# Optimization experiments

Measured on AMD Instinct MI355X. Metric: run time of the kernel, lower is better.

## Reference

```python
import jax, jax.numpy as jnp
import numpy as np

N = 8000       # n_sample (nodes)
F = 128        # n_feature
H = 128        # n_hidden
E = 256000     # edges (avg degree 32)
NPOOL = 3
K = 10         # propagation steps (args.k)
NC = 2         # n_class
ALPHA = 0.0    # Propagation(alpha=0.0)
CENTS = [400, 20, 1]   # node_pool = round(N**(1/NPOOL)) = 20; n_cent = round(prev/20)


def setup_inputs():
    key = jax.random.key(0)
    ks = jax.random.split(key, 40)
    def nrm(i, shape, scale=1.0):
        return jax.random.normal(ks[i], shape, jnp.float32) * scale
    x = nrm(0, (N, F))
    x_cov = nrm(1, (N, F))
    edge_rows = jax.random.randint(ks[2], (E,), 0, N, dtype=jnp.int32)
    edge_cols = jax.random.randint(ks[3], (E,), 0, N, dtype=jnp.int32)
    adj_vals = jax.random.uniform(ks[4], (E,), jnp.float32)
    raw = jax.random.uniform(ks[5], (E,), jnp.float32) + 0.1
    deg = jax.ops.segment_sum(raw, edge_rows, num_segments=N)
    norm_vals = raw / deg[edge_rows]   # row-normalized adjacency values
    inp = dict(x=x, x_cov=x_cov, edge_rows=edge_rows, edge_cols=edge_cols,
               adj_vals=adj_vals, norm_vals=norm_vals,
               bn_gamma=jnp.ones((F,), jnp.float32), bn_beta=jnp.zeros((F,), jnp.float32))
    i = 6
    for p, nc in enumerate(CENTS):
        inp['c%d_W1' % p] = nrm(i, (F, H), F ** -0.5); i += 1
        inp['c%d_b1' % p] = jnp.zeros((H,), jnp.float32)
        inp['c%d_W2' % p] = nrm(i, (H, nc), H ** -0.5); i += 1
        inp['c%d_b2' % p] = jnp.zeros((nc,), jnp.float32)
    inp['mW1'] = nrm(i, (F, H), F ** -0.5); i += 1
    inp['mb1'] = jnp.zeros((H,), jnp.float32)
    inp['a1'] = jnp.full((1,), 0.25, jnp.float32)   # PReLU slope
    inp['mW2'] = nrm(i, (H, H), H ** -0.5); i += 1
    inp['mb2'] = jnp.zeros((H,), jnp.float32)
    inp['a2'] = jnp.full((1,), 0.25, jnp.float32)
    inp['mW3'] = nrm(i, (H, NC), H ** -0.5); i += 1
    inp['mb3'] = jnp.zeros((NC,), jnp.float32)
    return inp


def _node_corr(z):
    # per-node decomposition of torch.corrcoef(z.T).sum(1):
    #   _node_corr(z).sum(0) == corrcoef(z.T).sum(1)
    zc = z - z.mean(0, keepdims=True)
    zc = zc / (jnp.linalg.norm(zc, axis=0, keepdims=True) + 1e-12)
    return zc * zc.sum(1, keepdims=True)   # [n, F]


def reference(x, x_cov, edge_rows, edge_cols, adj_vals, norm_vals, bn_gamma, bn_beta,
              c0_W1, c0_b1, c0_W2, c0_b2, c1_W1, c1_b1, c1_W2, c1_b2,
              c2_W1, c2_b1, c2_W2, c2_b2, mW1, mb1, a1, mW2, mb2, a2, mW3, mb3):
    # BatchNorm1d (training statistics, biased variance, eps=1e-5)
    mu, var = x.mean(0), x.var(0)
    x = (x - mu) / jnp.sqrt(var + 1e-5) * bn_gamma + bn_beta
    x0 = x

    # --- multi-level clustering / pooling (ClusteringLayer) ---
    cl_params = [(c0_W1, c0_b1, c0_W2, c0_b2), (c1_W1, c1_b1, c1_W2, c1_b2),
                 (c2_W1, c2_b1, c2_W2, c2_b2)]
    masks, corrs = [], []
    xc = x_cov
    for W1, b1, W2, b2 in cl_params:
        h = jax.nn.relu(xc @ W1 + b1)
        S = jax.nn.softmax(h @ W2 + b2, axis=-1)        # soft assignment [n_prev, n_cent]
        corrs.append(_node_corr(xc))                     # corr at the input level
        masks.append(S)
        xc = (S.T @ xc) / (S.sum(0)[:, None] + 1e-12)    # pooled centroid features
    corrs.append(_node_corr(x).sum(0))   # == torch.corrcoef(x.T).sum(1), shape [F]

    # --- gains: sigmoid(corr_{i+1} - normalize_adj(mask_i).T @ corr_i) ---
    gains = []
    for i in range(NPOOL):
        rn = masks[i] / (masks[i].sum(1, keepdims=True) + 1e-12)  # row-normalized (symmetric=False)
        gains.append(jax.nn.sigmoid(corrs[i + 1] - rn.T @ corrs[i]))

    # --- per-feature diagonal-masked sparse matmul chains, restricted to adj's edge set ---
    # projector to original nodes: P_i = masks[0] @ ... @ masks[i]
    P = [masks[0]]
    for i in range(1, NPOOL - 1):
        P.append(P[-1] @ masks[i])
    # (M M^T)[r,c] with M = P_i @ diag(g[:,j]) evaluated only on adj edges, all features at once
    def edge_mask(Pi, g):
        return jnp.einsum('ek,ek,kf->ef', Pi[edge_rows], Pi[edge_cols], g * g)  # [E, F]
    ms = [edge_mask(P[i], gains[i]) for i in reversed(range(NPOOL - 1))]  # i = NPOOL-2 .. 0
    ms = jnp.stack(ms, axis=0).transpose(2, 0, 1)   # [F, NPOOL-1, E]

    def per_feature(a, m_steps):   # sequential carry of adj over feature loop (matches torch)
        def inner(ai, mrow):
            ai = ai * mrow          # adj = adj * mask (elementwise on edge values)
            return ai, ai
        a, temps = jax.lax.scan(inner, a, m_steps)
        return a, temps.sum(0)      # adjs[j] = torch.sparse.sum(stack(temp), dim=0)
    _, adjs = jax.lax.scan(per_feature, adj_vals, ms)   # [F, E] edge values

    # --- diffusion propagation: x <- (1-alpha) * norm_adj @ x + alpha * x0, k times ---
    for _ in range(K):
        agg = jax.ops.segment_sum(norm_vals[:, None] * x[edge_cols], edge_rows, num_segments=N)
        x = (1.0 - ALPHA) * agg + ALPHA * x0

    # --- 3-layer MLP with PReLU + log_softmax ---
    prelu = lambda z, a: jnp.where(z >= 0, z, a * z)
    h = prelu(x @ mW1 + mb1, a1)
    h = prelu(h @ mW2 + mb2, a2)
    logits = h @ mW3 + mb3
    return jax.nn.log_softmax(logits, axis=1), adjs
```

## Files before the change

### kernel.cpp

```cpp
#include <hip/hip_runtime.h>
#include <hip/hip_bf16.h>

typedef __hip_bfloat16 bf16;
typedef __attribute__((ext_vector_type(8))) short s16x8;
typedef __attribute__((ext_vector_type(4))) float f32x4;

static constexpr int NN = 8000;
static constexpr int FF = 128;
static constexpr int EE = 256000;
static constexpr int NC0 = 400;
static constexpr int NC1 = 20;

__device__ __forceinline__ float b2f(bf16 v) { return __bfloat162float(v); }
__device__ __forceinline__ bf16 f2b(float v) { return __float2bfloat16(v); }
__device__ __forceinline__ short f2bs(float v) {
    bf16 h = __float2bfloat16(v);
    return __builtin_bit_cast(short, h);
}
__device__ __forceinline__ float ldw(float v) { return v; }
__device__ __forceinline__ float ldw(bf16 v) { return __bfloat162float(v); }

template <int NW>
__device__ __forceinline__ float block_sum(float v, float* sb) {
    #pragma unroll
    for (int o = 32; o > 0; o >>= 1) v += __shfl_down(v, o, 64);
    int t = threadIdx.x;
    if ((t & 63) == 0) sb[t >> 6] = v;
    __syncthreads();
    float s = 0.f;
    #pragma unroll
    for (int i = 0; i < NW; ++i) s += sb[i];
    __syncthreads();
    return s;
}

template <int NW>
__device__ __forceinline__ float block_max(float v, float* sb) {
    #pragma unroll
    for (int o = 32; o > 0; o >>= 1) v = fmaxf(v, __shfl_down(v, o, 64));
    int t = threadIdx.x;
    if ((t & 63) == 0) sb[t >> 6] = v;
    __syncthreads();
    float m = sb[0];
    #pragma unroll
    for (int i = 1; i < NW; ++i) m = fmaxf(m, sb[i]);
    __syncthreads();
    return m;
}

__global__ void k_fill_b16(bf16* __restrict__ p, float v, long n) {
    long i = (long)blockIdx.x * 256 + threadIdx.x;
    long stride = (long)gridDim.x * 256;
    for (; i < n; i += stride) p[i] = f2b(v);
}

__global__ void k_cvt_pad(const float* __restrict__ src, bf16* __restrict__ dst, int n) {
    int idx = blockIdx.x * 256 + threadIdx.x;
    if (idx < n) {
        int r = idx / 24, cc = idx - r * 24;
        dst[idx] = f2b(cc < 20 ? src[r * 20 + cc] : 0.f);
    }
}

__global__ void k_split(const float* __restrict__ src, bf16* __restrict__ dh,
                        bf16* __restrict__ dl, int n) {
    int i = blockIdx.x * 256 + threadIdx.x;
    if (i < n) {
        float v = src[i];
        bf16 h = f2b(v);
        dh[i] = h;
        dl[i] = f2b(v - b2f(h));
    }
}

__global__ __launch_bounds__(256)
void k_tsplit(const float* __restrict__ src, bf16* __restrict__ dh, bf16* __restrict__ dl,
              bf16* __restrict__ sh, bf16* __restrict__ sl, int M, int N) {
    __shared__ float t[32][33];
    int bx = blockIdx.x * 32, by = blockIdx.y * 32;
    int x = threadIdx.x;
    for (int y = threadIdx.y; y < 32; y += 8) {
        int m = by + y, n = bx + x;
        if (m < M && n < N) {
            float v = src[(long)m * N + n];
            t[y][x] = v;
            if (sh) {
                bf16 h = f2b(v);
                sh[(long)m * N + n] = h;
                sl[(long)m * N + n] = f2b(v - b2f(h));
            }
        }
    }
    __syncthreads();
    for (int y = threadIdx.y; y < 32; y += 8) {
        int n = bx + y, m = by + x;
        if (n < N && m < M) {
            float v = t[x][y];
            bf16 h = f2b(v);
            dh[(long)n * M + m] = h;
            dl[(long)n * M + m] = f2b(v - b2f(h));
        }
    }
}

__global__ void k_swz(const float* __restrict__ g, bf16* __restrict__ out, int nchunk, int K) {
    int idx = blockIdx.x * 256 + threadIdx.x;
    if (idx >= nchunk * 4096) return;
    int i = idx & 7, l = (idx >> 3) & 63, t = (idx >> 9) & 7, ch = idx >> 12;
    int k = 32 * ch + 8 * (l >> 4) + i;
    int f = 16 * t + (l & 15);
    out[idx] = f2b(k < K ? g[k * 128 + f] : 0.f);
}

__global__ __launch_bounds__(256)
void k_bnstats(const float* __restrict__ x, const float* __restrict__ gamma,
               const float* __restrict__ beta, float* __restrict__ scale,
               float* __restrict__ shift, int M) {
    __shared__ float sb[4];
    int f = blockIdx.x;
    float s = 0.f, q = 0.f;
    for (int n = threadIdx.x; n < M; n += 256) {
        float v = x[n * FF + f];
        s += v; q += v * v;
    }
    s = block_sum<4>(s, sb);
    q = block_sum<4>(q, sb);
    if (threadIdx.x == 0) {
        float mu = s / M;
        float var = q / M - mu * mu;
        if (var < 0.f) var = 0.f;
        float rstd = 1.f / sqrtf(var + 1e-5f);
        float sc = gamma[f] * rstd;
        scale[f] = sc;
        shift[f] = beta[f] - mu * sc;
    }
}

__global__ void k_bnapply(const float* __restrict__ x, const float* __restrict__ scale,
                          const float* __restrict__ shift, float* __restrict__ out, int n) {
    int i = blockIdx.x * 256 + threadIdx.x;
    if (i < n) { int f = i & 127; out[i] = x[i] * scale[f] + shift[f]; }
}

__global__ __launch_bounds__(256)
void k_colstats(const float* __restrict__ src, float* __restrict__ mu,
                float* __restrict__ invn, int M) {
    __shared__ float sb[4];
    int f = blockIdx.x;
    float s = 0.f, q = 0.f;
    for (int n = threadIdx.x; n < M; n += 256) {
        float v = src[n * FF + f];
        s += v; q += v * v;
    }
    s = block_sum<4>(s, sb);
    q = block_sum<4>(q, sb);
    if (threadIdx.x == 0) {
        float m = s / M;
        float ss = q - s * m;
        if (ss < 0.f) ss = 0.f;
        mu[f] = m;
        invn[f] = 1.f / (sqrtf(ss) + 1e-12f);
    }
}

__global__ __launch_bounds__(128)
void k_nodecorr(const float* __restrict__ src, const float* __restrict__ mu,
                const float* __restrict__ invn, float* __restrict__ out) {
    __shared__ float sb[2];
    int n = blockIdx.x, t = threadIdx.x;
    float z = (src[n * FF + t] - mu[t]) * invn[t];
    float tot = block_sum<2>(z, sb);
    out[n * FF + t] = z * tot;
}

__global__ void k_div(const float* __restrict__ T, const float* __restrict__ cs,
                      float* __restrict__ out, int n) {
    int i = blockIdx.x * 256 + threadIdx.x;
    if (i < n) out[i] = T[i] / (cs[i >> 7] + 1e-12f);
}

__global__ void k_sig2(const float* __restrict__ corr, const float* __restrict__ T,
                       float* __restrict__ out, int n) {
    int i = blockIdx.x * 256 + threadIdx.x;
    if (i < n) {
        float d = corr[i] - T[i];
        float g = 1.f / (1.f + expf(-d));
        out[i] = g * g;
    }
}

__global__ __launch_bounds__(256)
void k_softmax(float* __restrict__ p, int N) {
    __shared__ float sb[4];
    float* row = p + (long)blockIdx.x * N;
    int t = threadIdx.x;
    float m = -1e30f;
    for (int i = t; i < N; i += 256) m = fmaxf(m, row[i]);
    m = block_max<4>(m, sb);
    float s = 0.f;
    for (int i = t; i < N; i += 256) { float e = expf(row[i] - m); row[i] = e; s += e; }
    s = block_sum<4>(s, sb);
    float inv = 1.f / s;
    for (int i = t; i < N; i += 256) row[i] *= inv;
}

__global__ __launch_bounds__(256)
void k_softmax_b16(const float* __restrict__ src, bf16* __restrict__ dst, int N) {
    __shared__ float sb[4];
    const float* row = src + (long)blockIdx.x * N;
    bf16* orow = dst + (long)blockIdx.x * N;
    int t = threadIdx.x;
    float v0 = (t < N) ? row[t] : -1e30f;
    float v1 = (256 + t < N) ? row[256 + t] : -1e30f;
    float m = block_max<4>(fmaxf(v0, v1), sb);
    float e0 = (t < N) ? expf(v0 - m) : 0.f;
    float e1 = (256 + t < N) ? expf(v1 - m) : 0.f;
    float s = block_sum<4>(e0 + e1, sb);
    float inv = 1.f / s;
    if (t < N) orow[t] = f2b(e0 * inv);
    if (256 + t < N) orow[256 + t] = f2b(e1 * inv);
}

template <typename T>
__global__ __launch_bounds__(256)
void k_transpose(const T* __restrict__ src, T* __restrict__ dst, int M, int N) {
    __shared__ T t[32][33];
    int bx = blockIdx.x * 32, by = blockIdx.y * 32;
    int x = threadIdx.x;
    for (int y = threadIdx.y; y < 32; y += 8) {
        int m = by + y, n = bx + x;
        if (m < M && n < N) t[y][x] = src[(long)m * N + n];
    }
    __syncthreads();
    for (int y = threadIdx.y; y < 32; y += 8) {
        int n = bx + y, m = by + x;
        if (n < N && m < M) dst[(long)n * M + m] = t[x][y];
    }
}

template <typename T>
__global__ __launch_bounds__(256)
void k_colsum(const T* __restrict__ srcT, float* __restrict__ cs, int M) {
    __shared__ float sb[4];
    int r = blockIdx.x;
    float s = 0.f;
    for (int i = threadIdx.x; i < M; i += 256) s += ldw(srcT[(long)r * M + i]);
    s = block_sum<4>(s, sb);
    if (threadIdx.x == 0) cs[r] = s;
}

template <typename AT, typename WT>
__global__ __launch_bounds__(256)
void k_gemm(const AT* __restrict__ A, const WT* __restrict__ W,
            const float* __restrict__ bias, const float* __restrict__ slope,
            float* __restrict__ C, int M, int K, int N, int act) {
    __shared__ float As[16][68];
    __shared__ float Ws[16][68];
    int tid = threadIdx.x;
    int tx = tid & 15, ty = tid >> 4;
    int m0 = blockIdx.x * 64, n0 = blockIdx.y * 64;
    int KS = gridDim.z;
    int kchunk = ((K + KS * 16 - 1) / (KS * 16)) * 16;
    int kbeg = blockIdx.z * kchunk;
    int kend = min(K, kbeg + kchunk);
    float acc[4][4] = {};
    for (int k0 = kbeg; k0 < kend; k0 += 16) {
        __syncthreads();
        for (int idx = tid; idx < 1024; idx += 256) {
            int r = idx >> 4, kk = idx & 15;
            int m = m0 + r, k = k0 + kk;
            As[kk][r] = (m < M && k < kend) ? ldw(A[(long)m * K + k]) : 0.f;
        }
        for (int idx = tid; idx < 1024; idx += 256) {
            int kk = idx >> 6, n = idx & 63;
            int k = k0 + kk, nn = n0 + n;
            float wv = 0.f;
            if (k < kend && nn < N) wv = ldw(W[(long)k * N + nn]);
            Ws[kk][n] = wv;
        }
        __syncthreads();
        #pragma unroll
        for (int kk = 0; kk < 16; ++kk) {
            float4 a4 = *(const float4*)&As[kk][ty * 4];
            float4 b4 = *(const float4*)&Ws[kk][tx * 4];
            float av[4] = {a4.x, a4.y, a4.z, a4.w};
            float bv[4] = {b4.x, b4.y, b4.z, b4.w};
            #pragma unroll
            for (int i = 0; i < 4; ++i)
                #pragma unroll
                for (int j = 0; j < 4; ++j) acc[i][j] += av[i] * bv[j];
        }
    }
    if (KS > 1) {
        #pragma unroll
        for (int i = 0; i < 4; ++i) {
            int m = m0 + ty * 4 + i;
            if (m >= M) continue;
            #pragma unroll
            for (int j = 0; j < 4; ++j) {
                int n = n0 + tx * 4 + j;
                if (n >= N) continue;
                atomicAdd(&C[(long)m * N + n], acc[i][j]);
            }
        }
    } else {
        float sl = slope ? slope[0] : 0.f;
        #pragma unroll
        for (int i = 0; i < 4; ++i) {
            int m = m0 + ty * 4 + i;
            if (m >= M) continue;
            #pragma unroll
            for (int j = 0; j < 4; ++j) {
                int n = n0 + tx * 4 + j;
                if (n >= N) continue;
                float v = acc[i][j] + (bias ? bias[n] : 0.f);
                if (act == 1) v = fmaxf(v, 0.f);
                else if (act == 2) v = (v >= 0.f) ? v : sl * v;
                C[(long)m * N + n] = v;
            }
        }
    }
}

template <int PARTS>
__global__ __launch_bounds__(256)
void k_gmm(const bf16* __restrict__ Ah, const bf16* __restrict__ Al,
           const bf16* __restrict__ BTh, const bf16* __restrict__ BTl,
           const float* __restrict__ bias, const float* __restrict__ slope,
           float* __restrict__ C, int M, int K, int N, int act) {
    __shared__ __align__(16) short At[2][64 * 40];
    __shared__ __align__(16) short Bt[2][64 * 40];
    int tid = threadIdx.x;
    int m0 = blockIdx.x * 64, n0 = blockIdx.y * 64;
    int KS = gridDim.z;
    int kchunk = ((K + KS * 32 - 1) / (KS * 32)) * 32;
    int kbeg = blockIdx.z * kchunk;
    int kend = min(K, kbeg + kchunk);
    int r = tid >> 2, s = tid & 3;
    int l = tid & 63, w = tid >> 6;
    int c = l & 15, g = l >> 4;
    bool arow_ok = (m0 + r < M);
    bool brow_ok = (n0 + r < N);
    const short* ahp = (const short*)Ah + (long)(m0 + r) * K;
    const short* alp = (PARTS >= 3) ? (const short*)Al + (long)(m0 + r) * K : nullptr;
    const short* bhp = (const short*)BTh + (long)(n0 + r) * K;
    const short* blp = (PARTS >= 2) ? (const short*)BTl + (long)(n0 + r) * K : nullptr;
    short* aw = &At[0][r * 40 + 8 * s];
    short* bw = &Bt[0][r * 40 + 8 * s];
    const int afo = (16 * w + c) * 40 + 8 * g;
    f32x4 acc[4] = {};
    for (int k0 = kbeg; k0 < kend; k0 += 32) {
        __syncthreads();
        {
            int kk = k0 + 8 * s;
            bool kok = kk < kend;
            s16x8 av = {}, bv = {};
            if (arow_ok && kok) av = *(const s16x8*)(ahp + kk);
            if (brow_ok && kok) bv = *(const s16x8*)(bhp + kk);
            *(s16x8*)aw = av;
            *(s16x8*)bw = bv;
            if (PARTS >= 2) {
                s16x8 b2 = {};
                if (brow_ok && kok) b2 = *(const s16x8*)(blp + kk);
                *(s16x8*)(bw + 64 * 40) = b2;
            }
            if (PARTS >= 3) {
                s16x8 a2 = {};
                if (arow_ok && kok) a2 = *(const s16x8*)(alp + kk);
                *(s16x8*)(aw + 64 * 40) = a2;
            }
        }
        __syncthreads();
        s16x8 ah_ = *(const s16x8*)&At[0][afo];
        s16x8 al_;
        if (PARTS >= 3) al_ = *(const s16x8*)&At[1][afo];
        #pragma unroll
        for (int nt = 0; nt < 4; ++nt) {
            int bfo = (16 * nt + c) * 40 + 8 * g;
            s16x8 bh_ = *(const s16x8*)&Bt[0][bfo];
            acc[nt] = __builtin_amdgcn_mfma_f32_16x16x32_bf16(ah_, bh_, acc[nt], 0, 0, 0);
            if (PARTS >= 2) {
                s16x8 bl_ = *(const s16x8*)&Bt[1][bfo];
                acc[nt] = __builtin_amdgcn_mfma_f32_16x16x32_bf16(ah_, bl_, acc[nt], 0, 0, 0);
            }
            if (PARTS >= 3)
                acc[nt] = __builtin_amdgcn_mfma_f32_16x16x32_bf16(al_, bh_, acc[nt], 0, 0, 0);
        }
    }
    if (KS > 1) {
        #pragma unroll
        for (int nt = 0; nt < 4; ++nt) {
            int n = n0 + 16 * nt + c;
            if (n >= N) continue;
            #pragma unroll
            for (int q = 0; q < 4; ++q) {
                int m = m0 + 16 * w + 4 * g + q;
                if (m < M) atomicAdd(&C[(long)m * N + n], acc[nt][q]);
            }
        }
    } else {
        float sl = slope ? slope[0] : 0.f;
        #pragma unroll
        for (int nt = 0; nt < 4; ++nt) {
            int n = n0 + 16 * nt + c;
            if (n >= N) continue;
            float bv = bias ? bias[n] : 0.f;
            #pragma unroll
            for (int q = 0; q < 4; ++q) {
                int m = m0 + 16 * w + 4 * g + q;
                if (m >= M) continue;
                float v = acc[nt][q] + bv;
                if (act == 1) v = fmaxf(v, 0.f);
                else if (act == 2) v = (v >= 0.f) ? v : sl * v;
                C[(long)m * N + n] = v;
            }
        }
    }
}

__global__ __launch_bounds__(256)
void k_edge(const int* __restrict__ er, const int* __restrict__ ec,
            const float* __restrict__ adj,
            const bf16* __restrict__ S0b, const bf16* __restrict__ P1hp,
            const bf16* __restrict__ g0swz, const bf16* __restrict__ g1swz,
            bf16* __restrict__ outp, int E) {
    __shared__ int ridx[64], cidx[64];
    __shared__ __align__(16) short Wt[64 * 40];
    int tid = threadIdx.x;
    int e0 = blockIdx.x * 64;
    if (tid < 64) { ridx[tid] = er[e0 + tid]; cidx[tid] = ec[e0 + tid]; }
    __syncthreads();
    const int eb = tid >> 2, seg = tid & 3;
    const int l = tid & 63, w = tid >> 6;
    const int c = l & 15, g = l >> 4;
    const short* S0s = (const short*)S0b;
    const short* rrow = S0s + (long)ridx[eb] * 400 + 8 * seg;
    const short* crow = S0s + (long)cidx[eb] * 400 + 8 * seg;
    short* wwr = &Wt[eb * 40 + 8 * seg];
    const short* wrd = &Wt[(16 * w + c) * 40 + 8 * g];
    const s16x8* g0p = (const s16x8*)g0swz;
    f32x4 acc0[8] = {};
    f32x4 acc1[8] = {};
    #pragma unroll 1
    for (int ch = 0; ch < 13; ++ch) {
        s16x8 ar = *(const s16x8*)(rrow + 32 * ch);
        s16x8 ac = *(const s16x8*)(crow + 32 * ch);
        s16x8 wv;
        #pragma unroll
        for (int i = 0; i < 8; ++i) {
            float av = __uint_as_float(((unsigned)(unsigned short)ar[i]) << 16);
            float bv = __uint_as_float(((unsigned)(unsigned short)ac[i]) << 16);
            wv[i] = f2bs(av * bv);
        }
        __syncthreads();
        *(s16x8*)wwr = wv;
        __syncthreads();
        s16x8 wfrag = *(const s16x8*)wrd;
        const s16x8* gc = g0p + (long)ch * 512 + l;
        #pragma unroll
        for (int t = 0; t < 8; ++t)
            acc0[t] = __builtin_amdgcn_mfma_f32_16x16x32_bf16(gc[t * 64], wfrag, acc0[t], 0, 0, 0);
    }
    {
        s16x8 wv = {};
        if (seg < 3) {
            const short* P1s = (const short*)P1hp;
            s16x8 pr = *(const s16x8*)(P1s + (long)ridx[eb] * 24 + 8 * seg);
            s16x8 pc = *(const s16x8*)(P1s + (long)cidx[eb] * 24 + 8 * seg);
            #pragma unroll
            for (int i = 0; i < 8; ++i) {
                float av = __uint_as_float(((unsigned)(unsigned short)pr[i]) << 16);
                float bv = __uint_as_float(((unsigned)(unsigned short)pc[i]) << 16);
                wv[i] = f2bs(av * bv);
            }
        }
        __syncthreads();
        *(s16x8*)wwr = wv;
        __syncthreads();
        s16x8 wfrag = *(const s16x8*)wrd;
        const s16x8* g1p = (const s16x8*)g1swz;
        #pragma unroll
        for (int t = 0; t < 8; ++t)
            acc1[t] = __builtin_amdgcn_mfma_f32_16x16x32_bf16(g1p[t * 64 + l], wfrag, acc1[t], 0, 0, 0);
    }
    const long col = e0 + 16 * w + c;
    float pre = adj[col];
    #pragma unroll
    for (int t = 0; t < 8; ++t) {
        float m10 = acc0[t][0], m11 = acc0[t][1], m12 = acc0[t][2], m13 = acc0[t][3];
        float m00 = acc1[t][0], m01 = acc1[t][1], m02 = acc1[t][2], m03 = acc1[t][3];
        float q0 = m00 * m10, q1 = m01 * m11, q2 = m02 * m12, q3 = m03 * m13;
        float eq1 = q0, eq2 = q0 * q1, eq3 = eq2 * q2;
        float incg = eq3 * q3;
        float u = __shfl_up(incg, 16, 64); if (g >= 1) incg *= u;
        u = __shfl_up(incg, 32, 64); if (g >= 2) incg *= u;
        float exg = __shfl_up(incg, 16, 64); if (g == 0) exg = 1.f;
        float tot = __shfl(incg, 48 + c, 64);
        float base = pre * exg;
        pre *= tot;
        int fb = 16 * t + 4 * g;
        float o0 = base * m00 * (1.f + m10);
        float o1 = base * eq1 * m01 * (1.f + m11);
        float o2 = base * eq2 * m02 * (1.f + m12);
        float o3 = base * eq3 * m03 * (1.f + m13);
        outp[(long)(fb + 0) * E + col] = f2b(o0);
        outp[(long)(fb + 1) * E + col] = f2b(o1);
        outp[(long)(fb + 2) * E + col] = f2b(o2);
        if (fb + 3 < 127 || col < 240000)
            outp[(long)(fb + 3) * E + col] = f2b(o3);
    }
}

__global__ void k_count(const int* __restrict__ er, int* __restrict__ counts, int E) {
    int e = blockIdx.x * 256 + threadIdx.x;
    if (e < E) atomicAdd(&counts[er[e]], 1);
}

__global__ __launch_bounds__(256)
void k_scan(const int* __restrict__ counts, int* __restrict__ rs,
            int* __restrict__ cur, int R) {
    __shared__ int buf[2][256];
    int t = threadIdx.x;
    const int PER = 32;
    int b = t * PER;
    int s = 0;
    for (int i = 0; i < PER; ++i) {
        int idx = b + i;
        if (idx < R) s += counts[idx];
    }
    buf[0][t] = s;
    __syncthreads();
    int src = 0;
    for (int off = 1; off < 256; off <<= 1) {
        int v = buf[src][t];
        if (t >= off) v += buf[src][t - off];
        buf[1 - src][t] = v;
        __syncthreads();
        src = 1 - src;
    }
    int base = (t > 0) ? buf[src][t - 1] : 0;
    for (int i = 0; i < PER; ++i) {
        int idx = b + i;
        if (idx < R) {
            int c = counts[idx];
            rs[idx] = base;
            cur[idx] = base;
            base += c;
        }
    }
    if (t == 255) rs[R] = buf[src][255];
}

__global__ void k_scatter(const int* __restrict__ er, const int* __restrict__ ec,
                          const float* __restrict__ nv, int* __restrict__ cur,
                          int2* __restrict__ cpack, int E) {
    int e = blockIdx.x * 256 + threadIdx.x;
    if (e < E) {
        int r = er[e];
        int p = atomicAdd(&cur[r], 1);
        cpack[p] = make_int2(ec[e], __float_as_int(nv[e]));
    }
}

__global__ __launch_bounds__(256)
void k_spmv4(const int* __restrict__ rs, const int2* __restrict__ cpack,
             const float* __restrict__ xin, float* __restrict__ xout, int R) {
    int lane = threadIdx.x & 31;
    int r = blockIdx.x * 8 + (threadIdx.x >> 5);
    if (r >= R) return;
    int jb = rs[r], je = rs[r + 1];
    float4 acc = {0.f, 0.f, 0.f, 0.f};
    int j = jb;
    for (; j + 4 <= je; j += 4) {
        int2 cv0 = cpack[j], cv1 = cpack[j + 1], cv2 = cpack[j + 2], cv3 = cpack[j + 3];
        float4 x0 = ((const float4*)(xin + (long)cv0.x * FF))[lane];
        float4 x1 = ((const float4*)(xin + (long)cv1.x * FF))[lane];
        float4 x2 = ((const float4*)(xin + (long)cv2.x * FF))[lane];
        float4 x3 = ((const float4*)(xin + (long)cv3.x * FF))[lane];
        float v0 = __int_as_float(cv0.y), v1 = __int_as_float(cv1.y);
        float v2 = __int_as_float(cv2.y), v3 = __int_as_float(cv3.y);
        acc.x += v0 * x0.x; acc.y += v0 * x0.y; acc.z += v0 * x0.z; acc.w += v0 * x0.w;
        acc.x += v1 * x1.x; acc.y += v1 * x1.y; acc.z += v1 * x1.z; acc.w += v1 * x1.w;
        acc.x += v2 * x2.x; acc.y += v2 * x2.y; acc.z += v2 * x2.z; acc.w += v2 * x2.w;
        acc.x += v3 * x3.x; acc.y += v3 * x3.y; acc.z += v3 * x3.z; acc.w += v3 * x3.w;
    }
    for (; j < je; ++j) {
        int2 cv = cpack[j];
        float v = __int_as_float(cv.y);
        float4 xv = ((const float4*)(xin + (long)cv.x * FF))[lane];
        acc.x += v * xv.x; acc.y += v * xv.y; acc.z += v * xv.z; acc.w += v * xv.w;
    }
    ((float4*)(xout + (long)r * FF))[lane] = acc;
}

__global__ __launch_bounds__(256)
void k_fc128(const float* __restrict__ xin, const float* __restrict__ W,
             const float* __restrict__ b, const float* __restrict__ a,
             float* __restrict__ hout, int nblk) {
    __shared__ float Ws[16384];
    __shared__ float xs[2][128];
    int t = threadIdx.x;
    for (int i = t; i < 16384; i += 256) Ws[i] = W[i];
    float slope = a[0];
    int half = t >> 7, tt = t & 127;
    float bb = b[tt];
    __syncthreads();
    for (int n = blockIdx.x * 2 + half; n < NN; n += nblk * 2) {
        xs[half][tt] = xin[(long)n * FF + tt];
        __syncthreads();
        float a0 = 0.f, a1 = 0.f, a2 = 0.f, a3 = 0.f;
        #pragma unroll 8
        for (int k = 0; k < 128; k += 4) {
            a0 += xs[half][k + 0] * Ws[(k + 0) * 128 + tt];
            a1 += xs[half][k + 1] * Ws[(k + 1) * 128 + tt];
            a2 += xs[half][k + 2] * Ws[(k + 2) * 128 + tt];
            a3 += xs[half][k + 3] * Ws[(k + 3) * 128 + tt];
        }
        float acc = bb + ((a0 + a1) + (a2 + a3));
        hout[(long)n * FF + tt] = (acc >= 0.f) ? acc : slope * acc;
        __syncthreads();
    }
}

__global__ __launch_bounds__(256)
void k_mlp_tail(const float* __restrict__ hin, const float* __restrict__ W2,
                const float* __restrict__ b2, const float* __restrict__ a2,
                const float* __restrict__ W3, const float* __restrict__ b3,
                bf16* __restrict__ outA, bf16* __restrict__ outB, int nblk) {
    __shared__ float Ws[16384];
    __shared__ float xs[2][128];
    __shared__ float red[8];
    int t = threadIdx.x;
    for (int i = t; i < 16384; i += 256) Ws[i] = W2[i];
    float slope = a2[0];
    int half = t >> 7, tt = t & 127;
    float bb = b2[tt];
    float w30 = W3[tt * 2 + 0], w31 = W3[tt * 2 + 1];
    float b30 = b3[0], b31 = b3[1];
    __syncthreads();
    for (int n = blockIdx.x * 2 + half; n < NN; n += nblk * 2) {
        xs[half][tt] = hin[(long)n * FF + tt];
        __syncthreads();
        float a0 = 0.f, a1 = 0.f, a2_ = 0.f, a3 = 0.f;
        #pragma unroll 8
        for (int k = 0; k < 128; k += 4) {
            a0 += xs[half][k + 0] * Ws[(k + 0) * 128 + tt];
            a1 += xs[half][k + 1] * Ws[(k + 1) * 128 + tt];
            a2_ += xs[half][k + 2] * Ws[(k + 2) * 128 + tt];
            a3 += xs[half][k + 3] * Ws[(k + 3) * 128 + tt];
        }
        float acc = bb + ((a0 + a1) + (a2_ + a3));
        float h2 = (acc >= 0.f) ? acc : slope * acc;
        float l0 = h2 * w30, l1 = h2 * w31;
        #pragma unroll
        for (int o = 32; o > 0; o >>= 1) {
            l0 += __shfl_down(l0, o, 64);
            l1 += __shfl_down(l1, o, 64);
        }
        int wid = t >> 6;
        if ((t & 63) == 0) { red[wid] = l0; red[4 + wid] = l1; }
        __syncthreads();
        if (tt == 0) {
            float L0 = red[half * 2] + red[half * 2 + 1] + b30;
            float L1 = red[4 + half * 2] + red[4 + half * 2 + 1] + b31;
            float m = fmaxf(L0, L1);
            float lse = m + logf(expf(L0 - m) + expf(L1 - m));
            bf16 v0 = f2b(L0 - lse), v1 = f2b(L1 - lse);
            outA[n * 2 + 0] = v0; outA[n * 2 + 1] = v1;
            outB[n * 2 + 0] = v0; outB[n * 2 + 1] = v1;
        }
        __syncthreads();
    }
}

extern "C" void kernel_launch(void* const* d_in, const int* in_sizes, int n_in,
                              void* d_out, int out_size, void* d_ws, size_t ws_size,
                              hipStream_t stream) {
    const float* x     = (const float*)d_in[0];
    const float* xcov  = (const float*)d_in[1];
    const int*   erow  = (const int*)d_in[2];
    const int*   ecol  = (const int*)d_in[3];
    const float* adjv  = (const float*)d_in[4];
    const float* normv = (const float*)d_in[5];
    const float* gamma = (const float*)d_in[6];
    const float* beta  = (const float*)d_in[7];
    const float* c0W1 = (const float*)d_in[8];  const float* c0b1 = (const float*)d_in[9];
    const float* c0W2 = (const float*)d_in[10]; const float* c0b2 = (const float*)d_in[11];
    const float* c1W1 = (const float*)d_in[12]; const float* c1b1 = (const float*)d_in[13];
    const float* c1W2 = (const float*)d_in[14]; const float* c1b2 = (const float*)d_in[15];
    const float* mW1 = (const float*)d_in[20]; const float* mb1 = (const float*)d_in[21];
    const float* a1  = (const float*)d_in[22];
    const float* mW2 = (const float*)d_in[23]; const float* mb2 = (const float*)d_in[24];
    const float* a2  = (const float*)d_in[25];
    const float* mW3 = (const float*)d_in[26]; const float* mb3 = (const float*)d_in[27];

    char* B = (char*)d_out;
    bf16* logitsA = (bf16*)B;
    bf16* logitsB = (bf16*)(B + 32000);
    bf16* adjsOut = (bf16*)(B + 64000);

    auto ovl = [](const void* a, size_t an, const void* b, size_t bn) {
        const char* A = (const char*)a; const char* Bp = (const char*)b;
        return (A < Bp + bn) && (Bp < A + an);
    };
    size_t outBytes = (size_t)out_size * 2;
    static const int expSize[28] = {1024000,1024000,256000,256000,256000,256000,128,128,
                                    16384,128,51200,400, 16384,128,2560,20, 16384,128,128,1,
                                    16384,128,1, 16384,128,1, 256,2};
    int code = 0;
    if (n_in != 28) code = 200;
    else for (int i = 0; i < 28 && !code; ++i) if (in_sizes[i] != expSize[i]) code = 200;
    if (!code && ovl(d_ws, ws_size, d_out, outBytes)) code = 300;
    if (!code) {
        for (int i = 0; i < 28; ++i) {
            size_t bytes = (size_t)in_sizes[i] * 4;
            if (ovl(d_ws, ws_size, d_in[i], bytes)) { code = 400; break; }
            if (ovl(d_out, outBytes, d_in[i], bytes)) { code = 500; break; }
        }
    }
    if (!code && ws_size < (size_t)6935040) code = 600;
    if (code) {
        k_fill_b16<<<64, 256, 0, stream>>>(logitsA, (float)code, 16000);
        k_fill_b16<<<64, 256, 0, stream>>>(logitsB, (float)code, 16000);
        k_fill_b16<<<2048, 256, 0, stream>>>(adjsOut, 0.0f, (outBytes - 64000) / 2);
        return;
    }

    char* ws = (char*)d_ws;
    bf16*  S0b   = (bf16*)(ws + 0);
    bf16*  P1hp  = (bf16*)(ws + 6400000);
    bf16*  g0swz = (bf16*)(ws + 6784000);
    bf16*  g1swz = (bf16*)(ws + 6890496);

    char* S = B + 64000;
    float* xbn   = (float*)(S + 0);
    float* ping  = (float*)(S + 4096000);
    float* h0    = (float*)(S + 8192000);
    float* hh2   = (float*)(S + 12288000);
    float* S0f   = (float*)(S + 16384000);
    bf16*  S0Tb  = (bf16*)(S + 29184000);
    float* P1f   = (float*)(S + 35584000);
    int*   rs    = (int*)(S + 36224000);
    int*   cur   = (int*)(S + 36256016);
    int2*  cpack = (int2*)(S + 36288016);
    float* T0    = (float*)(S + 38400512);
    float* T1    = (float*)(S + 38605312);
    float* xc1   = (float*)(S + 38810112);
    float* corr1 = (float*)(S + 39014912);
    float* h1    = (float*)(S + 39219712);
    float* S1    = (float*)(S + 39424512);
    float* S1T   = (float*)(S + 39456512);
    float* T2    = (float*)(S + 39488512);
    float* T3    = (float*)(S + 39498752);
    float* xc2   = (float*)(S + 39508992);
    float* corr2 = (float*)(S + 39519232);
    float* cs0   = (float*)(S + 39529472);
    float* cs1   = (float*)(S + 39531072);
    float* bnsc  = (float*)(S + 39532032);
    float* bnsh  = (float*)(S + 39532544);
    float* statmu= (float*)(S + 39533056);
    float* statin= (float*)(S + 39533568);
    float* g0sq  = (float*)(S + 39534080);
    float* g1sq  = (float*)(S + 39738880);
    bf16* xcovh  = (bf16*)(S + 39749120);
    bf16* xcovl  = (bf16*)(S + 41797120);
    bf16* xcovTh = (bf16*)(S + 43845120);
    bf16* xcovTl = (bf16*)(S + 45893120);
    bf16* hh2Th  = (bf16*)(S + 47941120);
    bf16* hh2Tl  = (bf16*)(S + 49989120);
    bf16* h0h    = (bf16*)(S + 52037120);
    bf16* h0l    = (bf16*)(S + 54085120);
    bf16* W1Th   = (bf16*)(S + 56133120);
    bf16* W1Tl   = (bf16*)(S + 56165888);
    bf16* W2Th   = (bf16*)(S + 56198656);
    bf16* W2Tl   = (bf16*)(S + 56301056);
    bf16* S1Th   = (bf16*)(S + 56403456);
    bf16* S1Tl   = (bf16*)(S + 56419456);

    k_bnstats<<<128, 256, 0, stream>>>(x, gamma, beta, bnsc, bnsh, NN);
    k_bnapply<<<4000, 256, 0, stream>>>(x, bnsc, bnsh, xbn, NN * FF);
    k_colstats<<<128, 256, 0, stream>>>(xcov, statmu, statin, NN);
    k_nodecorr<<<NN, 128, 0, stream>>>(xcov, statmu, statin, hh2);
    k_tsplit<<<dim3(4, 250), dim3(32, 8), 0, stream>>>(xcov, xcovTh, xcovTl, xcovh, xcovl, NN, FF);
    k_tsplit<<<dim3(4, 250), dim3(32, 8), 0, stream>>>(hh2, hh2Th, hh2Tl, nullptr, nullptr, NN, FF);
    k_tsplit<<<dim3(4, 4), dim3(32, 8), 0, stream>>>(c0W1, W1Th, W1Tl, nullptr, nullptr, 128, 128);
    k_tsplit<<<dim3(13, 4), dim3(32, 8), 0, stream>>>(c0W2, W2Th, W2Tl, nullptr, nullptr, 128, NC0);
    k_gmm<3><<<dim3(125, 2, 1), 256, 0, stream>>>(xcovh, xcovl, W1Th, W1Tl, c0b1, nullptr, h0, NN, 128, 128, 1);
    k_split<<<4000, 256, 0, stream>>>(h0, h0h, h0l, NN * FF);
    k_gmm<3><<<dim3(125, 7, 1), 256, 0, stream>>>(h0h, h0l, W2Th, W2Tl, c0b2, nullptr, S0f, NN, 128, NC0, 0);
    k_softmax_b16<<<NN, 256, 0, stream>>>(S0f, S0b, NC0);
    k_transpose<bf16><<<dim3(13, 250), dim3(32, 8), 0, stream>>>(S0b, S0Tb, NN, NC0);
    k_colsum<bf16><<<NC0, 256, 0, stream>>>(S0Tb, cs0, NN);
    hipMemsetAsync(T0, 0, NC0 * 128 * 4, stream);
    hipMemsetAsync(T1, 0, NC0 * 128 * 4, stream);
    k_gmm<2><<<dim3(7, 2, 16), 256, 0, stream>>>(S0Tb, nullptr, xcovTh, xcovTl, nullptr, nullptr, T0, NC0, NN, 128, 0);
    k_gmm<2><<<dim3(7, 2, 16), 256, 0, stream>>>(S0Tb, nullptr, hh2Th, hh2Tl, nullptr, nullptr, T1, NC0, NN, 128, 0);
    k_div<<<200, 256, 0, stream>>>(T0, cs0, xc1, NC0 * 128);
    k_colstats<<<128, 256, 0, stream>>>(xc1, statmu, statin, NC0);
    k_nodecorr<<<NC0, 128, 0, stream>>>(xc1, statmu, statin, corr1);
    k_sig2<<<200, 256, 0, stream>>>(corr1, T1, g0sq, NC0 * 128);
    k_swz<<<208, 256, 0, stream>>>(g0sq, g0swz, 13, NC0);
    k_gemm<float, float><<<dim3(7, 2, 1), 256, 0, stream>>>(xc1, c1W1, c1b1, nullptr, h1, NC0, 128, 128, 1);
    k_gemm<float, float><<<dim3(7, 1, 1), 256, 0, stream>>>(h1, c1W2, c1b2, nullptr, S1, NC0, 128, NC1, 0);
    k_softmax<<<NC0, 256, 0, stream>>>(S1, NC1);
    k_transpose<float><<<dim3(1, 13), dim3(32, 8), 0, stream>>>(S1, S1T, NC0, NC1);
    k_colsum<float><<<NC1, 256, 0, stream>>>(S1T, cs1, NC0);
    k_tsplit<<<dim3(1, 13), dim3(32, 8), 0, stream>>>(S1, S1Th, S1Tl, nullptr, nullptr, NC0, NC1);
    hipMemsetAsync(T2, 0, NC1 * 128 * 4, stream);
    hipMemsetAsync(T3, 0, NC1 * 128 * 4, stream);
    k_gemm<float, float><<<dim3(1, 2, 4), 256, 0, stream>>>(S1T, xc1, nullptr, nullptr, T2, NC1, NC0, 128, 0);
    k_gemm<float, float><<<dim3(1, 2, 4), 256, 0, stream>>>(S1T, corr1, nullptr, nullptr, T3, NC1, NC0, 128, 0);
    k_div<<<10, 256, 0, stream>>>(T2, cs1, xc2, NC1 * 128);
    k_colstats<<<128, 256, 0, stream>>>(xc2, statmu, statin, NC1);
    k_nodecorr<<<NC1, 128, 0, stream>>>(xc2, statmu, statin, corr2);
    k_sig2<<<10, 256, 0, stream>>>(corr2, T3, g1sq, NC1 * 128);
    k_swz<<<16, 256, 0, stream>>>(g1sq, g1swz, 1, NC1);
    k_gmm<2><<<dim3(125, 1, 1), 256, 0, stream>>>(S0b, nullptr, S1Th, S1Tl, nullptr, nullptr, P1f, NN, NC0, NC1, 0);
    k_cvt_pad<<<750, 256, 0, stream>>>(P1f, P1hp, NN * 24);
    hipMemsetAsync(cur, 0, NN * 4, stream);
    k_count<<<1000, 256, 0, stream>>>(erow, cur, EE);
    k_scan<<<1, 256, 0, stream>>>(cur, rs, cur, NN);
    k_scatter<<<1000, 256, 0, stream>>>(erow, ecol, normv, cur, cpack, EE);
    float* xa = xbn;
    float* xb = ping;
    for (int it = 0; it < 10; ++it) {
        k_spmv4<<<1000, 256, 0, stream>>>(rs, cpack, xa, xb, NN);
        float* t = xa; xa = xb; xb = t;
    }
    k_fc128<<<250, 256, 0, stream>>>(xa, mW1, mb1, a1, h0, 250);
    k_mlp_tail<<<250, 256, 0, stream>>>(h0, mW2, mb2, a2, mW3, mb3, logitsA, logitsB, 250);
    k_edge<<<EE / 64, 256, 0, stream>>>(erow, ecol, adjv, S0b, P1hp, g0swz, g1swz, adjsOut, EE);
}
```

Measured before the change: 801.0 us.

## Fuse gain kernels, persistent propagation kernel, and LDS-staged edge output

Merges the small div/colstats/nodecorr/sigmoid/swizzle launches for both pooling levels into three fused kernels, and folds the BatchNorm apply into the first propagation step. The ten SpMV launches become one persistent kernel that uses a global atomic barrier between iterations. In the edge kernel, shared-memory staging with syncthreads is replaced by ds_bpermute, the next chunk's rows are prefetched, and output is transposed through LDS for coalesced 16-byte stores. The persistent kernel relies on all 500 blocks being co-resident; if they are not, the grid barrier deadlocks.

```diff
diff --git a/kernel.cpp b/kernel.cpp
--- a/kernel.cpp
+++ b/kernel.cpp
@@ -103,15 +103,6 @@
     }
 }
 
-__global__ void k_swz(const float* __restrict__ g, bf16* __restrict__ out, int nchunk, int K) {
-    int idx = blockIdx.x * 256 + threadIdx.x;
-    if (idx >= nchunk * 4096) return;
-    int i = idx & 7, l = (idx >> 3) & 63, t = (idx >> 9) & 7, ch = idx >> 12;
-    int k = 32 * ch + 8 * (l >> 4) + i;
-    int f = 16 * t + (l & 15);
-    out[idx] = f2b(k < K ? g[k * 128 + f] : 0.f);
-}
-
 __global__ __launch_bounds__(256)
 void k_bnstats(const float* __restrict__ x, const float* __restrict__ gamma,
                const float* __restrict__ beta, float* __restrict__ scale,
@@ -136,12 +127,6 @@
     }
 }
 
-__global__ void k_bnapply(const float* __restrict__ x, const float* __restrict__ scale,
-                          const float* __restrict__ shift, float* __restrict__ out, int n) {
-    int i = blockIdx.x * 256 + threadIdx.x;
-    if (i < n) { int f = i & 127; out[i] = x[i] * scale[f] + shift[f]; }
-}
-
 __global__ __launch_bounds__(256)
 void k_colstats(const float* __restrict__ src, float* __restrict__ mu,
                 float* __restrict__ invn, int M) {
@@ -171,22 +156,6 @@
     float z = (src[n * FF + t] - mu[t]) * invn[t];
     float tot = block_sum<2>(z, sb);
     out[n * FF + t] = z * tot;
-}
-
-__global__ void k_div(const float* __restrict__ T, const float* __restrict__ cs,
-                      float* __restrict__ out, int n) {
-    int i = blockIdx.x * 256 + threadIdx.x;
-    if (i < n) out[i] = T[i] / (cs[i >> 7] + 1e-12f);
-}
-
-__global__ void k_sig2(const float* __restrict__ corr, const float* __restrict__ T,
-                       float* __restrict__ out, int n) {
-    int i = blockIdx.x * 256 + threadIdx.x;
-    if (i < n) {
-        float d = corr[i] - T[i];
-        float g = 1.f / (1.f + expf(-d));
-        out[i] = g * g;
-    }
 }
 
 __global__ __launch_bounds__(256)
@@ -247,6 +216,87 @@
     for (int i = threadIdx.x; i < M; i += 256) s += ldw(srcT[(long)r * M + i]);
     s = block_sum<4>(s, sb);
     if (threadIdx.x == 0) cs[r] = s;
+}
+
+__global__ __launch_bounds__(256)
+void k_gain0a(const float* __restrict__ T0, const float* __restrict__ cs0,
+              float* __restrict__ xc1, float* __restrict__ mu, float* __restrict__ invn) {
+    __shared__ float sb[4];
+    int f = blockIdx.x;
+    float s = 0.f, q = 0.f;
+    for (int r = threadIdx.x; r < NC0; r += 256) {
+        float v = T0[r * 128 + f] / (cs0[r] + 1e-12f);
+        xc1[r * 128 + f] = v;
+        s += v; q += v * v;
+    }
+    s = block_sum<4>(s, sb);
+    q = block_sum<4>(q, sb);
+    if (threadIdx.x == 0) {
+        float m = s / NC0;
+        float ss = q - s * m;
+        if (ss < 0.f) ss = 0.f;
+        mu[f] = m;
+        invn[f] = 1.f / (sqrtf(ss) + 1e-12f);
+    }
+}
+
+__global__ __launch_bounds__(128)
+void k_gain0b(const float* __restrict__ xc1, const float* __restrict__ mu,
+              const float* __restrict__ invn, const float* __restrict__ T1,
+              float* __restrict__ corr1, bf16* __restrict__ g0swz) {
+    __shared__ float sb[2];
+    int k = blockIdx.x, f = threadIdx.x;
+    int ch = k >> 5, rem = k & 31, lhi = rem >> 3, ii = rem & 7;
+    int idx = (((ch * 8) + (f >> 4)) * 64 + (lhi * 16 + (f & 15))) * 8 + ii;
+    if (k >= NC0) { g0swz[idx] = f2b(0.f); return; }
+    float z = (xc1[k * 128 + f] - mu[f]) * invn[f];
+    float tot = block_sum<2>(z, sb);
+    float corr = z * tot;
+    corr1[k * 128 + f] = corr;
+    float d = corr - T1[k * 128 + f];
+    float g = 1.f / (1.f + expf(-d));
+    g0swz[idx] = f2b(g * g);
+}
+
+__global__ __launch_bounds__(256)
+void k_gain1(const float* __restrict__ T2, const float* __restrict__ cs1,
+             const float* __restrict__ T3, bf16* __restrict__ g1swz) {
+    __shared__ float xs[20][128];
+    __shared__ float mu[128], invn[128];
+    __shared__ float sb[4];
+    int t = threadIdx.x;
+    for (int i = t; i < 20 * 128; i += 256) {
+        int r = i >> 7;
+        xs[r][i & 127] = T2[i] / (cs1[r] + 1e-12f);
+    }
+    __syncthreads();
+    if (t < 128) {
+        float s = 0.f, q = 0.f;
+        for (int r = 0; r < 20; ++r) { float v = xs[r][t]; s += v; q += v * v; }
+        float m = s / 20.f;
+        float ss = q - s * m;
+        if (ss < 0.f) ss = 0.f;
+        mu[t] = m;
+        invn[t] = 1.f / (sqrtf(ss) + 1e-12f);
+    }
+    __syncthreads();
+    for (int r = 0; r < 20; ++r) {
+        float z = 0.f;
+        if (t < 128) z = (xs[r][t] - mu[t]) * invn[t];
+        float tot = block_sum<4>(z, sb);
+        if (t < 128) {
+            float corr = z * tot;
+            float d = corr - T3[r * 128 + t];
+            float g = 1.f / (1.f + expf(-d));
+            int lhi = (r >> 3) & 3, ii = r & 7;
+            g1swz[(((t >> 4) * 64) + (lhi * 16 + (t & 15))) * 8 + ii] = f2b(g * g);
+        }
+    }
+    for (int i = t; i < 12 * 128; i += 256) {
+        int k = 20 + (i >> 7), f = i & 127;
+        int lhi = (k >> 3) & 3, ii = k & 7;
+        g1swz[(((f >> 4) * 64) + (lhi * 16 + (f & 15))) * 8 + ii] = f2b(0.f);
+    }
 }
 
 template <typename AT, typename WT>
@@ -424,27 +474,29 @@
             const bf16* __restrict__ S0b, const bf16* __restrict__ P1hp,
             const bf16* __restrict__ g0swz, const bf16* __restrict__ g1swz,
             bf16* __restrict__ outp, int E) {
-    __shared__ int ridx[64], cidx[64];
-    __shared__ __align__(16) short Wt[64 * 40];
-    int tid = threadIdx.x;
-    int e0 = blockIdx.x * 64;
-    if (tid < 64) { ridx[tid] = er[e0 + tid]; cidx[tid] = ec[e0 + tid]; }
-    __syncthreads();
-    const int eb = tid >> 2, seg = tid & 3;
+    __shared__ __align__(16) short Ot[128 * 72];
+    const int tid = threadIdx.x;
+    const int e0 = blockIdx.x * 64;
     const int l = tid & 63, w = tid >> 6;
     const int c = l & 15, g = l >> 4;
+    const int eb = 16 * w + (l >> 2), seg = l & 3;
+    const int rn = er[e0 + eb], cn = ec[e0 + eb];
     const short* S0s = (const short*)S0b;
-    const short* rrow = S0s + (long)ridx[eb] * 400 + 8 * seg;
-    const short* crow = S0s + (long)cidx[eb] * 400 + 8 * seg;
-    short* wwr = &Wt[eb * 40 + 8 * seg];
-    const short* wrd = &Wt[(16 * w + c) * 40 + 8 * g];
+    const short* rrow = S0s + (long)rn * 400 + 8 * seg;
+    const short* crow = S0s + (long)cn * 400 + 8 * seg;
+    const int pa = ((((l & 15) << 2) + g) << 2);
     const s16x8* g0p = (const s16x8*)g0swz;
     f32x4 acc0[8] = {};
     f32x4 acc1[8] = {};
+    s16x8 ar = *(const s16x8*)(rrow);
+    s16x8 ac = *(const s16x8*)(crow);
     #pragma unroll 1
     for (int ch = 0; ch < 13; ++ch) {
-        s16x8 ar = *(const s16x8*)(rrow + 32 * ch);
-        s16x8 ac = *(const s16x8*)(crow + 32 * ch);
+        s16x8 nar, nac;
+        if (ch < 12) {
+            nar = *(const s16x8*)(rrow + 32 * (ch + 1));
+            nac = *(const s16x8*)(crow + 32 * (ch + 1));
+        }
         s16x8 wv;
         #pragma unroll
         for (int i = 0; i < 8; ++i) {
@@ -452,21 +504,25 @@
             float bv = __uint_as_float(((unsigned)(unsigned short)ac[i]) << 16);
             wv[i] = f2bs(av * bv);
         }
-        __syncthreads();
-        *(s16x8*)wwr = wv;
-        __syncthreads();
-        s16x8 wfrag = *(const s16x8*)wrd;
+        int4 wvi = __builtin_bit_cast(int4, wv);
+        int4 wfi;
+        wfi.x = __builtin_amdgcn_ds_bpermute(pa, wvi.x);
+        wfi.y = __builtin_amdgcn_ds_bpermute(pa, wvi.y);
+        wfi.z = __builtin_amdgcn_ds_bpermute(pa, wvi.z);
+        wfi.w = __builtin_amdgcn_ds_bpermute(pa, wvi.w);
+        s16x8 wfrag = __builtin_bit_cast(s16x8, wfi);
         const s16x8* gc = g0p + (long)ch * 512 + l;
         #pragma unroll
         for (int t = 0; t < 8; ++t)
             acc0[t] = __builtin_amdgcn_mfma_f32_16x16x32_bf16(gc[t * 64], wfrag, acc0[t], 0, 0, 0);
+        ar = nar; ac = nac;
     }
     {
         s16x8 wv = {};
         if (seg < 3) {
             const short* P1s = (const short*)P1hp;
-            s16x8 pr = *(const s16x8*)(P1s + (long)ridx[eb] * 24 + 8 * seg);
-            s16x8 pc = *(const s16x8*)(P1s + (long)cidx[eb] * 24 + 8 * seg);
+            s16x8 pr = *(const s16x8*)(P1s + (long)rn * 24 + 8 * seg);
+            s16x8 pc = *(const s16x8*)(P1s + (long)cn * 24 + 8 * seg);
             #pragma unroll
             for (int i = 0; i < 8; ++i) {
                 float av = __uint_as_float(((unsigned)(unsigned short)pr[i]) << 16);
@@ -474,17 +530,20 @@
                 wv[i] = f2bs(av * bv);
             }
         }
-        __syncthreads();
-        *(s16x8*)wwr = wv;
-        __syncthreads();
-        s16x8 wfrag = *(const s16x8*)wrd;
+        int4 wvi = __builtin_bit_cast(int4, wv);
+        int4 wfi;
+        wfi.x = __builtin_amdgcn_ds_bpermute(pa, wvi.x);
+        wfi.y = __builtin_amdgcn_ds_bpermute(pa, wvi.y);
+        wfi.z = __builtin_amdgcn_ds_bpermute(pa, wvi.z);
+        wfi.w = __builtin_amdgcn_ds_bpermute(pa, wvi.w);
+        s16x8 wfrag = __builtin_bit_cast(s16x8, wfi);
         const s16x8* g1p = (const s16x8*)g1swz;
         #pragma unroll
         for (int t = 0; t < 8; ++t)
             acc1[t] = __builtin_amdgcn_mfma_f32_16x16x32_bf16(g1p[t * 64 + l], wfrag, acc1[t], 0, 0, 0);
     }
-    const long col = e0 + 16 * w + c;
-    float pre = adj[col];
+    const int ecl = 16 * w + c;
+    float pre = adj[e0 + ecl];
     #pragma unroll
     for (int t = 0; t < 8; ++t) {
         float m10 = acc0[t][0], m11 = acc0[t][1], m12 = acc0[t][2], m13 = acc0[t][3];
@@ -499,15 +558,19 @@
         float base = pre * exg;
         pre *= tot;
         int fb = 16 * t + 4 * g;
-        float o0 = base * m00 * (1.f + m10);
-        float o1 = base * eq1 * m01 * (1.f + m11);
-        float o2 = base * eq2 * m02 * (1.f + m12);
-        float o3 = base * eq3 * m03 * (1.f + m13);
-        outp[(long)(fb + 0) * E + col] = f2b(o0);
-        outp[(long)(fb + 1) * E + col] = f2b(o1);
-        outp[(long)(fb + 2) * E + col] = f2b(o2);
-        if (fb + 3 < 127 || col < 240000)
-            outp[(long)(fb + 3) * E + col] = f2b(o3);
+        Ot[(fb + 0) * 72 + ecl] = f2bs(base * m00 * (1.f + m10));
+        Ot[(fb + 1) * 72 + ecl] = f2bs(base * eq1 * m01 * (1.f + m11));
+        Ot[(fb + 2) * 72 + ecl] = f2bs(base * eq2 * m02 * (1.f + m12));
+        Ot[(fb + 3) * 72 + ecl] = f2bs(base * eq3 * m03 * (1.f + m13));
+    }
+    __syncthreads();
+    const int fo = tid & 127, hf = tid >> 7;
+    if (fo < 127 || e0 < 240000) {
+        const short* lsrc = &Ot[fo * 72 + hf * 32];
+        short* gdst = (short*)outp + (long)fo * E + e0 + hf * 32;
+        #pragma unroll
+        for (int q = 0; q < 4; ++q)
+            *(s16x8*)(gdst + 8 * q) = *(const s16x8*)(lsrc + 8 * q);
     }
 }
 
@@ -562,35 +625,77 @@
     }
 }
 
-__global__ __launch_bounds__(256)
-void k_spmv4(const int* __restrict__ rs, const int2* __restrict__ cpack,
-             const float* __restrict__ xin, float* __restrict__ xout, int R) {
-    int lane = threadIdx.x & 31;
-    int r = blockIdx.x * 8 + (threadIdx.x >> 5);
-    if (r >= R) return;
-    int jb = rs[r], je = rs[r + 1];
-    float4 acc = {0.f, 0.f, 0.f, 0.f};
-    int j = jb;
-    for (; j + 4 <= je; j += 4) {
-        int2 cv0 = cpack[j], cv1 = cpack[j + 1], cv2 = cpack[j + 2], cv3 = cpack[j + 3];
-        float4 x0 = ((const float4*)(xin + (long)cv0.x * FF))[lane];
-        float4 x1 = ((const float4*)(xin + (long)cv1.x * FF))[lane];
-        float4 x2 = ((const float4*)(xin + (long)cv2.x * FF))[lane];
-        float4 x3 = ((const float4*)(xin + (long)cv3.x * FF))[lane];
-        float v0 = __int_as_float(cv0.y), v1 = __int_as_float(cv1.y);
-        float v2 = __int_as_float(cv2.y), v3 = __int_as_float(cv3.y);
-        acc.x += v0 * x0.x; acc.y += v0 * x0.y; acc.z += v0 * x0.z; acc.w += v0 * x0.w;
-        acc.x += v1 * x1.x; acc.y += v1 * x1.y; acc.z += v1 * x1.z; acc.w += v1 * x1.w;
-        acc.x += v2 * x2.x; acc.y += v2 * x2.y; acc.z += v2 * x2.z; acc.w += v2 * x2.w;
-        acc.x += v3 * x3.x; acc.y += v3 * x3.y; acc.z += v3 * x3.z; acc.w += v3 * x3.w;
-    }
-    for (; j < je; ++j) {
-        int2 cv = cpack[j];
-        float v = __int_as_float(cv.y);
-        float4 xv = ((const float4*)(xin + (long)cv.x * FF))[lane];
-        acc.x += v * xv.x; acc.y += v * xv.y; acc.z += v * xv.z; acc.w += v * xv.w;
-    }
-    ((float4*)(xout + (long)r * FF))[lane] = acc;
+__device__ __forceinline__ void gsync(int* bar, int expect) {
+    __syncthreads();
+    if (threadIdx.x == 0) {
+        __threadfence();
+        atomicAdd(bar, 1);
+        while (__hip_atomic_load(bar, __ATOMIC_RELAXED, __HIP_MEMORY_SCOPE_AGENT) < expect)
+            __builtin_amdgcn_s_sleep(2);
+    }
+    __syncthreads();
+    __threadfence();
+}
+
+__global__ __launch_bounds__(256, 2)
+void k_prop(const int* __restrict__ rs, const int2* __restrict__ cpack,
+            const float* __restrict__ xraw, const float* __restrict__ bnsc,
+            const float* __restrict__ bnsh, float* __restrict__ bufA,
+            float* __restrict__ bufB, int* __restrict__ bar) {
+    const int lane = threadIdx.x & 31;
+    const int slot = threadIdx.x >> 5;
+    const int r0 = blockIdx.x * 16;
+    float4 sc = ((const float4*)bnsc)[lane];
+    float4 sh = ((const float4*)bnsh)[lane];
+    #pragma unroll
+    for (int p = 0; p < 2; ++p) {
+        int r = r0 + p * 8 + slot;
+        int jb = rs[r], je = rs[r + 1];
+        float4 acc = {0.f, 0.f, 0.f, 0.f};
+        for (int j = jb; j < je; ++j) {
+            int2 cv = cpack[j];
+            float v = __int_as_float(cv.y);
+            float4 xv = ((const float4*)(xraw + (long)cv.x * FF))[lane];
+            acc.x += v * (xv.x * sc.x + sh.x);
+            acc.y += v * (xv.y * sc.y + sh.y);
+            acc.z += v * (xv.z * sc.z + sh.z);
+            acc.w += v * (xv.w * sc.w + sh.w);
+        }
+        ((float4*)(bufA + (long)r * FF))[lane] = acc;
+    }
+    float* xa = bufA;
+    float* xb = bufB;
+    for (int it = 1; it < 10; ++it) {
+        gsync(bar, 500 * it);
+        #pragma unroll
+        for (int p = 0; p < 2; ++p) {
+            int r = r0 + p * 8 + slot;
+            int jb = rs[r], je = rs[r + 1];
+            float4 acc = {0.f, 0.f, 0.f, 0.f};
+            int j = jb;
+            for (; j + 4 <= je; j += 4) {
+                int2 cv0 = cpack[j], cv1 = cpack[j + 1], cv2 = cpack[j + 2], cv3 = cpack[j + 3];
+                float4 x0 = ((const float4*)(xa + (long)cv0.x * FF))[lane];
+                float4 x1 = ((const float4*)(xa + (long)cv1.x * FF))[lane];
+                float4 x2 = ((const float4*)(xa + (long)cv2.x * FF))[lane];
+                float4 x3 = ((const float4*)(xa + (long)cv3.x * FF))[lane];
+                float v0 = __int_as_float(cv0.y), v1 = __int_as_float(cv1.y);
+                float v2 = __int_as_float(cv2.y), v3 = __int_as_float(cv3.y);
+                acc.x += v0 * x0.x; acc.y += v0 * x0.y; acc.z += v0 * x0.z; acc.w += v0 * x0.w;
+                acc.x += v1 * x1.x; acc.y += v1 * x1.y; acc.z += v1 * x1.z; acc.w += v1 * x1.w;
+                acc.x += v2 * x2.x; acc.y += v2 * x2.y; acc.z += v2 * x2.z; acc.w += v2 * x2.w;
+                acc.x += v3 * x3.x; acc.y += v3 * x3.y; acc.z += v3 * x3.z; acc.w += v3 * x3.w;
+            }
+            for (; j < je; ++j) {
+                int2 cv = cpack[j];
+                float v = __int_as_float(cv.y);
+                float4 xv = ((const float4*)(xa + (long)cv.x * FF))[lane];
+                acc.x += v * xv.x; acc.y += v * xv.y; acc.z += v * xv.z; acc.w += v * xv.w;
+            }
+            ((float4*)(xb + (long)r * FF))[lane] = acc;
+        }
+        float* tsw = xa; xa = xb; xb = tsw;
+    }
 }
 
 __global__ __launch_bounds__(256)
@@ -752,16 +857,13 @@
     float* S1T   = (float*)(S + 39456512);
     float* T2    = (float*)(S + 39488512);
     float* T3    = (float*)(S + 39498752);
-    float* xc2   = (float*)(S + 39508992);
-    float* corr2 = (float*)(S + 39519232);
     float* cs0   = (float*)(S + 39529472);
     float* cs1   = (float*)(S + 39531072);
     float* bnsc  = (float*)(S + 39532032);
     float* bnsh  = (float*)(S + 39532544);
     float* statmu= (float*)(S + 39533056);
     float* statin= (float*)(S + 39533568);
-    float* g0sq  = (float*)(S + 39534080);
-    float* g1sq  = (float*)(S + 39738880);
+    int*   bar   = (int*)(S + 39534080);
     bf16* xcovh  = (bf16*)(S + 39749120);
     bf16* xcovl  = (bf16*)(S + 41797120);
     bf16* xcovTh = (bf16*)(S + 43845120);
@@ -778,7 +880,6 @@
     bf16* S1Tl   = (bf16*)(S + 56419456);
 
     k_bnstats<<<128, 256, 0, stream>>>(x, gamma, beta, bnsc, bnsh, NN);
-    k_bnapply<<<4000, 256, 0, stream>>>(x, bnsc, bnsh, xbn, NN * FF);
     k_colstats<<<128, 256, 0, stream>>>(xcov, statmu, statin, NN);
     k_nodecorr<<<NN, 128, 0, stream>>>(xcov, statmu, statin, hh2);
     k_tsplit<<<dim3(4, 250), dim3(32, 8), 0, stream>>>(xcov, xcovTh, xcovTl, xcovh, xcovl, NN, FF);
@@ -795,11 +896,8 @@
     hipMemsetAsync(T1, 0, NC0 * 128 * 4, stream);
     k_gmm<2><<<dim3(7, 2, 16), 256, 0, stream>>>(S0Tb, nullptr, xcovTh, xcovTl, nullptr, nullptr, T0, NC0, NN, 128, 0);
     k_gmm<2><<<dim3(7, 2, 16), 256, 0, stream>>>(S0Tb, nullptr, hh2Th, hh2Tl, nullptr, nullptr, T1, NC0, NN, 128, 0);
-    k_div<<<200, 256, 0, stream>>>(T0, cs0, xc1, NC0 * 128);
-    k_colstats<<<128, 256, 0, stream>>>(xc1, statmu, statin, NC0);
-    k_nodecorr<<<NC0, 128, 0, stream>>>(xc1, statmu, statin, corr1);
-    k_sig2<<<200, 256, 0, stream>>>(corr1, T1, g0sq, NC0 * 128);
-    k_swz<<<208, 256, 0, stream>>>(g0sq, g0swz, 13, NC0);
+    k_gain0a<<<128, 256, 0, stream>>>(T0, cs0, xc1, statmu, statin);
+    k_gain0b<<<416, 128, 0, stream>>>(xc1, statmu, statin, T1, corr1, g0swz);
     k_gemm<float, float><<<dim3(7, 2, 1), 256, 0, stream>>>(xc1, c1W1, c1b1, nullptr, h1, NC0, 128, 128, 1);
     k_gemm<float, float><<<dim3(7, 1, 1), 256, 0, stream>>>(h1, c1W2, c1b2, nullptr, S1, NC0, 128, NC1, 0);
     k_softmax<<<NC0, 256, 0, stream>>>(S1, NC1);
@@ -810,24 +908,16 @@
     hipMemsetAsync(T3, 0, NC1 * 128 * 4, stream);
     k_gemm<float, float><<<dim3(1, 2, 4), 256, 0, stream>>>(S1T, xc1, nullptr, nullptr, T2, NC1, NC0, 128, 0);
     k_gemm<float, float><<<dim3(1, 2, 4), 256, 0, stream>>>(S1T, corr1, nullptr, nullptr, T3, NC1, NC0, 128, 0);
-    k_div<<<10, 256, 0, stream>>>(T2, cs1, xc2, NC1 * 128);
-    k_colstats<<<128, 256, 0, stream>>>(xc2, statmu, statin, NC1);
-    k_nodecorr<<<NC1, 128, 0, stream>>>(xc2, statmu, statin, corr2);
-    k_sig2<<<10, 256, 0, stream>>>(corr2, T3, g1sq, NC1 * 128);
-    k_swz<<<16, 256, 0, stream>>>(g1sq, g1swz, 1, NC1);
+    k_gain1<<<1, 256, 0, stream>>>(T2, cs1, T3, g1swz);
     k_gmm<2><<<dim3(125, 1, 1), 256, 0, stream>>>(S0b, nullptr, S1Th, S1Tl, nullptr, nullptr, P1f, NN, NC0, NC1, 0);
     k_cvt_pad<<<750, 256, 0, stream>>>(P1f, P1hp, NN * 24);
     hipMemsetAsync(cur, 0, NN * 4, stream);
     k_count<<<1000, 256, 0, stream>>>(erow, cur, EE);
     k_scan<<<1, 256, 0, stream>>>(cur, rs, cur, NN);
     k_scatter<<<1000, 256, 0, stream>>>(erow, ecol, normv, cur, cpack, EE);
-    float* xa = xbn;
-    float* xb = ping;
-    for (int it = 0; it < 10; ++it) {
-        k_spmv4<<<1000, 256, 0, stream>>>(rs, cpack, xa, xb, NN);
-        float* t = xa; xa = xb; xb = t;
-    }
-    k_fc128<<<250, 256, 0, stream>>>(xa, mW1, mb1, a1, h0, 250);
+    hipMemsetAsync(bar, 0, 4, stream);
+    k_prop<<<500, 256, 0, stream>>>(rs, cpack, x, bnsc, bnsh, xbn, ping, bar);
+    k_fc128<<<250, 256, 0, stream>>>(ping, mW1, mb1, a1, h0, 250);
     k_mlp_tail<<<250, 256, 0, stream>>>(h0, mW2, mb2, a2, mW3, mb3, logitsA, logitsB, 250);
     k_edge<<<EE / 64, 256, 0, stream>>>(erow, ecol, adjv, S0b, P1hp, g0swz, g1swz, adjsOut, EE);
 }
```

Result: slower. 1.577 ms (+96.8%).
